# Optimization experiments

Hardware: AMD Instinct MI355X
Metric: run time of the kernel (lower is better)

The kernel has to match this reference:

```python
import jax, jax.numpy as jnp
import numpy as np

K = 16  # nsample for knn_point

def _bn(x, g, b):
    # inference-mode BatchNorm1d folded to per-channel affine (running stats 0/1)
    return x * g[None, :, None] + b[None, :, None]

def _knn(xyz, k):
    # xyz: [B,3,N] -> idx [B,N,k] of k nearest neighbors (squared L2)
    p = xyz.transpose(0, 2, 1)                                   # [B,N,3]
    sq = jnp.sum(p * p, axis=-1)                                 # [B,N]
    d = sq[:, :, None] + sq[:, None, :] - 2.0 * jnp.einsum('bnc,bmc->bnm', p, p)
    _, idx = jax.lax.top_k(-d, k)
    return idx

def _gather(hT, idx):
    # hT: [B,N,C], idx: [B,N,K] -> [B,N,K,C]
    return jax.vmap(lambda a, i: a[i])(hT, idx)

def setup_inputs():
    key = jax.random.key(0)
    ks = jax.random.split(key, 12)
    B, N, C = 16, 2048, 128
    def w(k, shape, fan):
        return jax.random.normal(k, shape, jnp.float32) * (1.0 / np.sqrt(fan))
    o = jnp.ones; z = jnp.zeros
    return {
        'points': jax.random.normal(ks[0], (B, 6, N), jnp.float32),
        'label': jax.random.uniform(ks[1], (B, 1, 16), jnp.float32),
        'We1': w(ks[2], (C, 6), 6), 'ge1': o(C), 'be1': z(C),
        'We2': w(ks[3], (C, C), C), 'ge2': o(C), 'be2': z(C),
        'W1': w(ks[4], (3, C, C), C), 'g1': o((3, C)), 'b1': z((3, C)),
        'W2': w(ks[5], (3, C, C), C), 'g2': o((3, C)), 'b2': z((3, C)),
        'Wf': w(ks[6], (1024, 3 * C), 3 * C), 'gf': o(1024), 'bf': z(1024),
        'Wl': w(ks[7], (64, 16), 16), 'gl': o(64), 'bl': z(64),
        'Wc1': w(ks[8], (512, 3136), 3136), 'bc1': z(512), 'gc1': o(512), 'bb1': z(512),
        'Wc2': w(ks[9], (256, 512), 512), 'bc2': z(256), 'gc2': o(256), 'bb2': z(256),
        'Wc3': w(ks[10], (50, 256), 256), 'bc3': z(50),
    }

def reference(points, label, We1, ge1, be1, We2, ge2, be2, W1, g1, b1, W2, g2, b2,
              Wf, gf, bf, Wl, gl, bl, Wc1, bc1, gc1, bb1, Wc2, bc2, gc2, bb2, Wc3, bc3):
    B, _, N = points.shape
    x = points[:, :6, :]
    xyz = x[:, :3, :]
    idx = _knn(xyz, K)                                            # [B,N,16]
    # input embedding: two conv1x1 + BN + ReLU
    h = jax.nn.relu(_bn(jnp.einsum('oc,bcn->bon', We1, x), ge1, be1))
    h = jax.nn.relu(_bn(jnp.einsum('oc,bcn->bon', We2, h), ge2, be2))
    xs = []
    for i in range(3):  # PVDSA_Res blocks (simplified: conv-BN-ReLU, kNN max-agg, conv-BN + residual)
        t = jax.nn.relu(_bn(jnp.einsum('oc,bcn->bon', W1[i], h), g1[i], b1[i]))
        nbr = _gather(t.transpose(0, 2, 1), idx)                  # [B,N,K,C]
        m = nbr.max(axis=2).transpose(0, 2, 1)                    # [B,C,N]
        h = jax.nn.relu(_bn(jnp.einsum('oc,bcn->bon', W2[i], m), g2[i], b2[i]) + h)
        xs.append(h)
    xcat = jnp.concatenate(xs, axis=1)                            # [B,384,N]
    xf = jax.nn.leaky_relu(_bn(jnp.einsum('oc,bcn->bon', Wf, xcat), gf, bf), 0.2)  # [B,1024,N]
    x_max = xf.max(axis=-1)                                       # [B,1024]
    x_avg = xf.mean(axis=-1)                                      # [B,1024]
    cls = jnp.broadcast_to(label.transpose(0, 2, 1), (B, 16, N))
    lab = jax.nn.leaky_relu(_bn(jnp.einsum('oc,bcn->bon', Wl, cls), gl, bl), 0.2)  # [B,64,N]
    glob = jnp.concatenate([
        jnp.broadcast_to(x_max[:, :, None], (B, 1024, N)),
        jnp.broadcast_to(x_avg[:, :, None], (B, 1024, N)),
        lab], axis=1)
    xa = jnp.concatenate([xf, glob], axis=1)                      # [B,3136,N]
    c = jax.nn.relu(_bn(jnp.einsum('oc,bcn->bon', Wc1, xa) + bc1[None, :, None], gc1, bb1))
    c = jax.nn.relu(_bn(jnp.einsum('oc,bcn->bon', Wc2, c) + bc2[None, :, None], gc2, bb2))
    out = jnp.einsum('oc,bcn->bon', Wc3, c) + bc3[None, :, None]  # [B,50,N]
    return out
```

## Files before the change

kernel.cpp:

```cpp
#include <hip/hip_runtime.h>
#include <cstdint>
#include <cstddef>

#define DEVINL __device__ __forceinline__

typedef float    f32x4 __attribute__((ext_vector_type(4)));
typedef _Float16 f16x8 __attribute__((ext_vector_type(8)));
typedef _Float16 f16x4 __attribute__((ext_vector_type(4)));

constexpr int BB = 16, NN = 2048, MM = 32768;

constexpr size_t OFF_WE1 = 0;
constexpr size_t OFF_WE2 = OFF_WE1 + 128 * 64 * 2;
constexpr size_t OFF_W1  = OFF_WE2 + 128 * 128 * 2;
constexpr size_t OFF_W2  = OFF_W1  + 3 * 128 * 128 * 2;
constexpr size_t OFF_WF  = OFF_W2  + 3 * 128 * 128 * 2;
constexpr size_t OFF_WC1 = OFF_WF  + 1024 * 384 * 2;
constexpr size_t OFF_WC2 = OFF_WC1 + 512 * 1024 * 2;
constexpr size_t OFF_WC3 = OFF_WC2 + 256 * 512 * 2;
constexpr size_t OFF_BC2 = OFF_WC3 + 128 * 256 * 2;
constexpr size_t OFF_BC3 = OFF_BC2 + 256 * 4;
constexpr size_t OFF_CVEC= OFF_BC3 + 128 * 4;
constexpr size_t OFF_PMAX= OFF_CVEC+ 16 * 512 * 4;
constexpr size_t OFF_PSUM= OFF_PMAX+ 16 * 16 * 1024 * 4;
constexpr size_t OFF_IDX = OFF_PSUM+ 16 * 16 * 1024 * 4;
constexpr size_t OFF_R1  = 8ull << 20;
constexpr size_t OFF_X0  = OFF_R1;
constexpr size_t OFF_HT  = OFF_R1 + (4ull  << 20);
constexpr size_t OFF_TT  = OFF_R1 + (12ull << 20);
constexpr size_t OFF_MT  = OFF_R1 + (20ull << 20);
constexpr size_t OFF_C1  = OFF_R1;
constexpr size_t OFF_XCAT= OFF_R1 + (32ull << 20);
constexpr size_t OFF_C2  = OFF_XCAT;
constexpr size_t OFF_XF  = OFF_XCAT + (24ull << 20);

__global__ __launch_bounds__(256) void fold_all_kernel(
    const float* We1, const float* ge1, const float* We2, const float* ge2,
    const float* W1,  const float* g1,  const float* W2,  const float* g2,
    const float* Wf,  const float* gf,  const float* Wc1, const float* gc1,
    const float* Wc2, const float* gc2, const float* Wc3,
    const float* gc2b, const float* bc2, const float* bb2, const float* bc3,
    const float* pts, char* ws)
{
    const int bid = blockIdx.x;
    const int tid = threadIdx.x;

    if (bid == 4704) {
        ((float*)(ws + OFF_BC2))[tid] = gc2b[tid] * bc2[tid] + bb2[tid];
        return;
    }
    if (bid == 4705) {
        if (tid < 128) ((float*)(ws + OFF_BC3))[tid] = (tid < 50) ? bc3[tid] : 0.f;
        return;
    }
    if (bid >= 4706) {
        int m = (bid - 4706) * 256 + tid;
        int b = m >> 11, n = m & 2047;
        const float* ps = pts + (size_t)b * 6 * 2048 + n;
        _Float16 tmp[64];
#pragma unroll
        for (int c = 0; c < 64; ++c) tmp[c] = (_Float16)0.f;
#pragma unroll
        for (int c = 0; c < 6; ++c) tmp[c] = (_Float16)ps[(size_t)c << 11];
        _Float16* dst = (_Float16*)(ws + OFF_X0) + (size_t)m * 64;
#pragma unroll
        for (int v = 0; v < 8; ++v) *(f16x8*)(dst + v * 8) = *(const f16x8*)(tmp + v * 8);
        return;
    }

    int id, base;
    if      (bid < 32)   { id = 0;  base = 0;    }
    else if (bid < 96)   { id = 1;  base = 32;   }
    else if (bid < 160)  { id = 2;  base = 96;   }
    else if (bid < 224)  { id = 3;  base = 160;  }
    else if (bid < 288)  { id = 4;  base = 224;  }
    else if (bid < 352)  { id = 5;  base = 288;  }
    else if (bid < 416)  { id = 6;  base = 352;  }
    else if (bid < 480)  { id = 7;  base = 416;  }
    else if (bid < 2016) { id = 8;  base = 480;  }
    else if (bid < 4064) { id = 9;  base = 2016; }
    else if (bid < 4576) { id = 10; base = 4064; }
    else                 { id = 11; base = 4576; }

    const float* src = nullptr; const float* g = nullptr; _Float16* dst = nullptr;
    int O = 0, K = 0, lds = 0, Kp = 0;
    switch (id) {
        case 0:  src = We1; g = ge1; O = 128; K = 6;    lds = 6;    Kp = 64;   dst = (_Float16*)(ws + OFF_WE1); break;
        case 1:  src = We2; g = ge2; O = 128; K = 128;  lds = 128;  Kp = 128;  dst = (_Float16*)(ws + OFF_WE2); break;
        case 2: case 3: case 4: {
            int i = id - 2;
            src = W1 + (size_t)i * 16384; g = g1 + i * 128; O = 128; K = 128; lds = 128; Kp = 128;
            dst = (_Float16*)(ws + OFF_W1) + (size_t)i * 16384; break; }
        case 5: case 6: case 7: {
            int i = id - 5;
            src = W2 + (size_t)i * 16384; g = g2 + i * 128; O = 128; K = 128; lds = 128; Kp = 128;
            dst = (_Float16*)(ws + OFF_W2) + (size_t)i * 16384; break; }
        case 8:  src = Wf;  g = gf;  O = 1024; K = 384;  lds = 384;  Kp = 384;  dst = (_Float16*)(ws + OFF_WF);  break;
        case 9:  src = Wc1; g = gc1; O = 512;  K = 1024; lds = 3136; Kp = 1024; dst = (_Float16*)(ws + OFF_WC1); break;
        case 10: src = Wc2; g = gc2; O = 256;  K = 512;  lds = 512;  Kp = 512;  dst = (_Float16*)(ws + OFF_WC2); break;
        default: src = Wc3; g = nullptr; O = 50; K = 256; lds = 256; Kp = 256;  dst = (_Float16*)(ws + OFF_WC3); break;
    }
    int e = (bid - base) * 256 + tid;
    int o = e / Kp, k = e - o * Kp;
    float v = 0.f;
    if (o < O && k < K) {
        v = src[(size_t)o * lds + k];
        if (g) v *= g[o];
    }
    dst[e] = (_Float16)v;
}

DEVINL float knn_dist(const float4 pq, const float4 pm) {
    float t = pq.x * pm.x;
    t = fmaf(pq.y, pm.y, t);
    t = fmaf(pq.z, pm.z, t);
    return fmaf(-2.f, t, pm.w);
}

#define KNN_DINS(X) do { \
    const float x_ = (X); \
    d15 = __builtin_amdgcn_fmed3f(x_, d14, d15); \
    d14 = __builtin_amdgcn_fmed3f(x_, d13, d14); \
    d13 = __builtin_amdgcn_fmed3f(x_, d12, d13); \
    d12 = __builtin_amdgcn_fmed3f(x_, d11, d12); \
    d11 = __builtin_amdgcn_fmed3f(x_, d10, d11); \
    d10 = __builtin_amdgcn_fmed3f(x_, d9,  d10); \
    d9  = __builtin_amdgcn_fmed3f(x_, d8,  d9);  \
    d8  = __builtin_amdgcn_fmed3f(x_, d7,  d8);  \
    d7  = __builtin_amdgcn_fmed3f(x_, d6,  d7);  \
    d6  = __builtin_amdgcn_fmed3f(x_, d5,  d6);  \
    d5  = __builtin_amdgcn_fmed3f(x_, d4,  d5);  \
    d4  = __builtin_amdgcn_fmed3f(x_, d3,  d4);  \
    d3  = __builtin_amdgcn_fmed3f(x_, d2,  d3);  \
    d2  = __builtin_amdgcn_fmed3f(x_, d1,  d2);  \
    d1  = __builtin_amdgcn_fmed3f(x_, d0,  d1);  \
    d0  = __builtin_amdgcn_fmed3f(x_, -3.4e38f, d0); \
} while (0)

#define KNN_CE(A, B) { const float lo_ = fminf(A, B), hi_ = fmaxf(A, B); A = lo_; B = hi_; }

#define KNN_MERGE(OFF) do { \
    const float n0  = __shfl_xor(d0,  OFF), n1  = __shfl_xor(d1,  OFF), \
                n2  = __shfl_xor(d2,  OFF), n3  = __shfl_xor(d3,  OFF), \
                n4  = __shfl_xor(d4,  OFF), n5  = __shfl_xor(d5,  OFF), \
                n6  = __shfl_xor(d6,  OFF), n7  = __shfl_xor(d7,  OFF), \
                n8  = __shfl_xor(d8,  OFF), n9  = __shfl_xor(d9,  OFF), \
                n10 = __shfl_xor(d10, OFF), n11 = __shfl_xor(d11, OFF), \
                n12 = __shfl_xor(d12, OFF), n13 = __shfl_xor(d13, OFF), \
                n14 = __shfl_xor(d14, OFF), n15 = __shfl_xor(d15, OFF); \
    d0  = fminf(d0,  n15); d1  = fminf(d1,  n14); d2  = fminf(d2,  n13); d3  = fminf(d3,  n12); \
    d4  = fminf(d4,  n11); d5  = fminf(d5,  n10); d6  = fminf(d6,  n9);  d7  = fminf(d7,  n8);  \
    d8  = fminf(d8,  n7);  d9  = fminf(d9,  n6);  d10 = fminf(d10, n5);  d11 = fminf(d11, n4);  \
    d12 = fminf(d12, n3);  d13 = fminf(d13, n2);  d14 = fminf(d14, n1);  d15 = fminf(d15, n0);  \
    KNN_CE(d0, d8)  KNN_CE(d1, d9)  KNN_CE(d2, d10) KNN_CE(d3, d11) \
    KNN_CE(d4, d12) KNN_CE(d5, d13) KNN_CE(d6, d14) KNN_CE(d7, d15) \
    KNN_CE(d0, d4)  KNN_CE(d1, d5)  KNN_CE(d2, d6)  KNN_CE(d3, d7)  \
    KNN_CE(d8, d12) KNN_CE(d9, d13) KNN_CE(d10,d14) KNN_CE(d11,d15) \
    KNN_CE(d0, d2)  KNN_CE(d1, d3)  KNN_CE(d4, d6)  KNN_CE(d5, d7)  \
    KNN_CE(d8, d10) KNN_CE(d9, d11) KNN_CE(d12,d14) KNN_CE(d13,d15) \
    KNN_CE(d0, d1)  KNN_CE(d2, d3)  KNN_CE(d4, d5)  KNN_CE(d6, d7)  \
    KNN_CE(d8, d9)  KNN_CE(d10,d11) KNN_CE(d12,d13) KNN_CE(d14,d15) \
} while (0)

__global__ __launch_bounds__(256) void knn_kernel(const float* __restrict__ pts, int* __restrict__ idxout)
{
    __shared__ float4 P[2048];
    __shared__ unsigned short buf[32][96];
    __shared__ int cnt[32];
    __shared__ int wcnt[32];
    const int tid = threadIdx.x;
    const int b = blockIdx.x;
    const float* pb = pts + (size_t)b * 6 * 2048;
    for (int i = tid; i < 2048; i += 256) {
        float x = pb[i];
        float y = pb[2048 + i];
        float z = pb[4096 + i];
        P[i] = make_float4(x, y, z, x * x + y * y + z * z);
    }
    if (tid < 32) { cnt[tid] = 0; wcnt[tid] = 0; }
    __syncthreads();

    const int p = tid & 7;
    const int g = tid >> 3;
    const int q = blockIdx.y * 32 + g;
    const float4 pq = P[q];

    float d0 = 3.4e38f, d1 = 3.4e38f, d2 = 3.4e38f, d3 = 3.4e38f;
#pragma unroll 4
    for (int it = 0; it < 256; ++it) {
        const float4 pm = P[it * 8 + p];
        const float x = knn_dist(pq, pm);
        d3 = __builtin_amdgcn_fmed3f(x, d2, d3);
        d2 = __builtin_amdgcn_fmed3f(x, d1, d2);
        d1 = __builtin_amdgcn_fmed3f(x, d0, d1);
        d0 = fminf(x, d0);
    }
    float d4 = 3.4e38f, d5 = 3.4e38f, d6 = 3.4e38f, d7 = 3.4e38f,
          d8 = 3.4e38f, d9 = 3.4e38f, d10 = 3.4e38f, d11 = 3.4e38f,
          d12 = 3.4e38f, d13 = 3.4e38f, d14 = 3.4e38f, d15 = 3.4e38f;
    KNN_MERGE(1);
    KNN_MERGE(2);
    KNN_MERGE(4);
    const float tub = d15;

#pragma unroll 4
    for (int it = 0; it < 256; ++it) {
        const int m = it * 8 + p;
        const float d = knn_dist(pq, P[m]);
        if (d <= tub) {
            const int pos = atomicAdd(&cnt[g], 1);
            if (pos < 96) buf[g][pos] = (unsigned short)m;
        }
    }
    int C = cnt[g];
    if (C > 96) C = 96;

    d0 = 3.4e38f; d1 = 3.4e38f; d2 = 3.4e38f; d3 = 3.4e38f;
    d4 = 3.4e38f; d5 = 3.4e38f; d6 = 3.4e38f; d7 = 3.4e38f;
    d8 = 3.4e38f; d9 = 3.4e38f; d10 = 3.4e38f; d11 = 3.4e38f;
    d12 = 3.4e38f; d13 = 3.4e38f; d14 = 3.4e38f; d15 = 3.4e38f;
    for (int j = p; j < C; j += 8) {
        const int m = buf[g][j];
        const float x = knn_dist(pq, P[m]);
        KNN_DINS(x);
    }
    KNN_MERGE(1);
    KNN_MERGE(2);
    KNN_MERGE(4);
    const float t = d15;

    int* op = idxout + (((size_t)(b << 11) + q) << 4);
    for (int j = p; j < C; j += 8) {
        const int m = buf[g][j];
        const float d = knn_dist(pq, P[m]);
        if (d <= t) {
            const int pos = atomicAdd(&wcnt[g], 1);
            if (pos < 16) op[pos] = m;
        }
    }
}

__global__ __launch_bounds__(256) void e12_kernel(
    const _Float16* __restrict__ W1e, const _Float16* __restrict__ W2e,
    const _Float16* __restrict__ X, _Float16* __restrict__ Y,
    const float* __restrict__ b1v, const float* __restrict__ b2v)
{
    __shared__ _Float16 SH[36864];
    _Float16* A1s = SH;
    _Float16* B1s = SH + 8192;
    _Float16* A2s = SH + 12288;
    _Float16* B2s = SH + 28672;

    const int tid = threadIdx.x;
    const int lane = tid & 63, wave = tid >> 6;
    const int r = lane & 15, quad = lane >> 4;
    const int m_blk = blockIdx.x * 64;
    const int oh = (wave >> 1) * 64, mh = (wave & 1) * 32;

    const int srow  = wave * 8 + (lane >> 3);
    const int sslot = lane & 7;

#pragma unroll
    for (int t = 0; t < 4; ++t) {
        const int row = t * 32 + srow;
        const int gk = (sslot ^ (row & 7)) << 3;
        __builtin_amdgcn_global_load_lds(
            (const __attribute__((address_space(1))) unsigned int*)(W1e + (size_t)row * 64 + gk),
            (__attribute__((address_space(3))) unsigned int*)(A1s + t * 2048 + wave * 512),
            16, 0, 0);
    }
#pragma unroll
    for (int t = 0; t < 2; ++t) {
        const int row = t * 32 + srow;
        const int gk = (sslot ^ (row & 7)) << 3;
        __builtin_amdgcn_global_load_lds(
            (const __attribute__((address_space(1))) unsigned int*)(X + (size_t)(m_blk + row) * 64 + gk),
            (__attribute__((address_space(3))) unsigned int*)(B1s + t * 2048 + wave * 512),
            16, 0, 0);
    }
#pragma unroll
    for (int kt = 0; kt < 2; ++kt)
#pragma unroll
        for (int t = 0; t < 4; ++t) {
            const int row = t * 32 + srow;
            const int gk = kt * 64 + ((sslot ^ (row & 7)) << 3);
            __builtin_amdgcn_global_load_lds(
                (const __attribute__((address_space(1))) unsigned int*)(W2e + (size_t)row * 128 + gk),
                (__attribute__((address_space(3))) unsigned int*)(A2s + kt * 8192 + t * 2048 + wave * 512),
                16, 0, 0);
        }

    asm volatile("s_waitcnt vmcnt(8)" ::: "memory");
    __builtin_amdgcn_sched_barrier(0);
    __builtin_amdgcn_s_barrier();
    asm volatile("" ::: "memory");

    f32x4 acc1[4][2];
#pragma unroll
    for (int a = 0; a < 4; ++a)
#pragma unroll
        for (int c = 0; c < 2; ++c) acc1[a][c] = (f32x4){0.f, 0.f, 0.f, 0.f};
#pragma unroll
    for (int ks = 0; ks < 2; ++ks) {
        f16x8 af[4], bf[2];
#pragma unroll
        for (int oi = 0; oi < 4; ++oi) {
            const int row = oh + oi * 16 + r;
            const int slot = (ks * 4 + quad) ^ (row & 7);
            af[oi] = *(const f16x8*)(A1s + row * 64 + slot * 8);
        }
#pragma unroll
        for (int mi = 0; mi < 2; ++mi) {
            const int row = mh + mi * 16 + r;
            const int slot = (ks * 4 + quad) ^ (row & 7);
            bf[mi] = *(const f16x8*)(B1s + row * 64 + slot * 8);
        }
#pragma unroll
        for (int oi = 0; oi < 4; ++oi)
#pragma unroll
            for (int mi = 0; mi < 2; ++mi)
                acc1[oi][mi] = __builtin_amdgcn_mfma_f32_16x16x32_f16(af[oi], bf[mi], acc1[oi][mi], 0, 0, 0);
    }

#pragma unroll
    for (int oi = 0; oi < 4; ++oi) {
        const int ob = oh + oi * 16 + quad * 4;
        const f32x4 bv = *(const f32x4*)(b1v + ob);
        const int kt = ob >> 6, kk = ob & 63;
        const int chunk = kk >> 3, within = kk & 7;
#pragma unroll
        for (int mi = 0; mi < 2; ++mi) {
            const int row = mh + mi * 16 + r;
            f32x4 v = acc1[oi][mi] + bv;
            f16x4 ov;
#pragma unroll
            for (int j = 0; j < 4; ++j) { float x = v[j]; ov[j] = (_Float16)((x > 0.f) ? x : 0.f); }
            *(f16x4*)(B2s + kt * 4096 + row * 64 + ((chunk ^ (row & 7)) << 3) + within) = ov;
        }
    }
    __syncthreads();

    f32x4 acc2[4][2];
#pragma unroll
    for (int a = 0; a < 4; ++a)
#pragma unroll
        for (int c = 0; c < 2; ++c) acc2[a][c] = (f32x4){0.f, 0.f, 0.f, 0.f};
#pragma unroll
    for (int kt = 0; kt < 2; ++kt)
#pragma unroll
        for (int ks = 0; ks < 2; ++ks) {
            f16x8 af[4], bf[2];
#pragma unroll
            for (int oi = 0; oi < 4; ++oi) {
                const int row = oh + oi * 16 + r;
                const int slot = (ks * 4 + quad) ^ (row & 7);
                af[oi] = *(const f16x8*)(A2s + kt * 8192 + row * 64 + slot * 8);
            }
#pragma unroll
            for (int mi = 0; mi < 2; ++mi) {
                const int row = mh + mi * 16 + r;
                const int slot = (ks * 4 + quad) ^ (row & 7);
                bf[mi] = *(const f16x8*)(B2s + kt * 4096 + row * 64 + slot * 8);
            }
#pragma unroll
            for (int oi = 0; oi < 4; ++oi)
#pragma unroll
                for (int mi = 0; mi < 2; ++mi)
                    acc2[oi][mi] = __builtin_amdgcn_mfma_f32_16x16x32_f16(af[oi], bf[mi], acc2[oi][mi], 0, 0, 0);
        }
    __syncthreads();

    _Float16* OT = SH;
#pragma unroll
    for (int oi = 0; oi < 4; ++oi) {
        const int ol = oh + oi * 16 + quad * 4;
        const f32x4 bv = *(const f32x4*)(b2v + ol);
#pragma unroll
        for (int mi = 0; mi < 2; ++mi) {
            const int row = mh + mi * 16 + r;
            f32x4 v = acc2[oi][mi] + bv;
            f16x4 ov;
#pragma unroll
            for (int j = 0; j < 4; ++j) { float x = v[j]; ov[j] = (_Float16)((x > 0.f) ? x : 0.f); }
            const int s = ((ol >> 2) ^ (row & 31)) << 2;
            *(f16x4*)(OT + row * 128 + s) = ov;
        }
    }
    __syncthreads();
#pragma unroll
    for (int it2 = 0; it2 < 4; ++it2) {
        const int row = it2 * 16 + (tid >> 4);
        const int c = tid & 15;
        const int s0 = ((c * 2) ^ (row & 31)) << 2;
        const int s1 = ((c * 2 + 1) ^ (row & 31)) << 2;
        f16x4 a  = *(const f16x4*)(OT + row * 128 + s0);
        f16x4 b2 = *(const f16x4*)(OT + row * 128 + s1);
        f16x8 o8;
        o8[0] = a[0]; o8[1] = a[1]; o8[2] = a[2]; o8[3] = a[3];
        o8[4] = b2[0]; o8[5] = b2[1]; o8[6] = b2[2]; o8[7] = b2[3];
        *(f16x8*)(Y + (size_t)(m_blk + row) * 128 + c * 8) = o8;
    }
}

__global__ __launch_bounds__(512, 2) void gemm256(
    const _Float16* __restrict__ W, const _Float16* __restrict__ X,
    _Float16* __restrict__ Y, const float* __restrict__ bias,
    int Kp, int ldX, int ldY, int Opad, int act, int biasPerBatch,
    float* __restrict__ pmax, float* __restrict__ psum)
{
    constexpr int ASZ = 256 * 64;
    __shared__ _Float16 SH[65536];
    const int tid  = threadIdx.x;
    const int lane = tid & 63, wave = tid >> 6;
    const int r = lane & 15, quad = lane >> 4;
    const int wo = wave & 3, wm = wave >> 2;
    const int m_blk = blockIdx.x * 256, o_blk = blockIdx.y * 256;
    const int nt = Kp >> 6;

    f32x4 acc[4][8];
#pragma unroll
    for (int a = 0; a < 4; ++a)
#pragma unroll
        for (int c = 0; c < 8; ++c) acc[a][c] = (f32x4){0.f, 0.f, 0.f, 0.f};

    const int srow  = wave * 8 + (lane >> 3);
    const int sslot = lane & 7;

    auto STAGE = [&](int bufi, int k0) {
        _Float16* As = SH + bufi * (2 * ASZ);
        _Float16* Bs = As + ASZ;
#pragma unroll
        for (int t = 0; t < 4; ++t) {
            const int rowA = t * 64 + srow;
            const int gk = k0 + ((sslot ^ (rowA & 7)) << 3);
            const _Float16* gA = W + (size_t)(o_blk + rowA) * Kp + gk;
            __builtin_amdgcn_global_load_lds(
                (const __attribute__((address_space(1))) unsigned int*)gA,
                (__attribute__((address_space(3))) unsigned int*)(As + t * 4096 + wave * 512),
                16, 0, 0);
        }
#pragma unroll
        for (int t = 0; t < 4; ++t) {
            const int rowB = t * 64 + srow;
            const int gk = k0 + ((sslot ^ (rowB & 7)) << 3);
            const _Float16* gB = X + (size_t)(m_blk + rowB) * ldX + gk;
            __builtin_amdgcn_global_load_lds(
                (const __attribute__((address_space(1))) unsigned int*)gB,
                (__attribute__((address_space(3))) unsigned int*)(Bs + t * 4096 + wave * 512),
                16, 0, 0);
        }
    };

    STAGE(0, 0);
    int cur = 0;
    for (int t = 0; t < nt; ++t) {
        if (t + 1 < nt) {
            STAGE(cur ^ 1, (t + 1) << 6);
            asm volatile("s_waitcnt vmcnt(8)" ::: "memory");
        } else {
            asm volatile("s_waitcnt vmcnt(0)" ::: "memory");
        }
        __builtin_amdgcn_sched_barrier(0);
        __builtin_amdgcn_s_barrier();
        asm volatile("" ::: "memory");

        const _Float16* As = SH + cur * (2 * ASZ);
        const _Float16* Bs = As + ASZ;
        __builtin_amdgcn_s_setprio(1);
#pragma unroll
        for (int ks = 0; ks < 2; ++ks) {
            f16x8 af[4], bf[8];
#pragma unroll
            for (int oi = 0; oi < 4; ++oi) {
                const int row = (wo << 6) + (oi << 4) + r;
                const int slot = (ks * 4 + quad) ^ (row & 7);
                af[oi] = *(const f16x8*)(As + row * 64 + slot * 8);
            }
#pragma unroll
            for (int mi = 0; mi < 8; ++mi) {
                const int row = (wm << 7) + (mi << 4) + r;
                const int slot = (ks * 4 + quad) ^ (row & 7);
                bf[mi] = *(const f16x8*)(Bs + row * 64 + slot * 8);
            }
#pragma unroll
            for (int oi = 0; oi < 4; ++oi)
#pragma unroll
                for (int mi = 0; mi < 8; ++mi)
                    acc[oi][mi] = __builtin_amdgcn_mfma_f32_16x16x32_f16(af[oi], bf[mi], acc[oi][mi], 0, 0, 0);
        }
        __builtin_amdgcn_s_setprio(0);
        asm volatile("" ::: "memory");
        __builtin_amdgcn_s_barrier();
        cur ^= 1;
    }
    __syncthreads();

    const int bb = biasPerBatch ? (m_blk >> 11) * Opad : 0;
    _Float16* OT = SH;
#pragma unroll
    for (int oi = 0; oi < 4; ++oi) {
        const int ol = (wo << 6) + (oi << 4) + (quad << 2);
        const f32x4 bv = *(const f32x4*)(bias + bb + o_blk + ol);
#pragma unroll
        for (int mi = 0; mi < 8; ++mi) {
            const int row = (wm << 7) + (mi << 4) + r;
            f32x4 v = acc[oi][mi] + bv;
            f16x4 ov;
#pragma unroll
            for (int j = 0; j < 4; ++j) {
                float x = v[j];
                if (act == 1)      x = (x > 0.f) ? x : 0.0f;
                else if (act == 2) x = (x > 0.f) ? x : 0.2f * x;
                ov[j] = (_Float16)x;
            }
            const int s = (ol >> 2) ^ (row & 31);
            *(f16x4*)(OT + row * 256 + s * 4) = ov;
        }
    }
    __syncthreads();
#pragma unroll
    for (int p2 = 0; p2 < 16; ++p2) {
        const int g = (p2 << 9) + tid;
        const int row = g >> 5, c = g & 31;
        const int s0 = ((c << 1)) ^ (row & 31);
        const int s1 = ((c << 1) | 1) ^ (row & 31);
        f16x4 a  = *(const f16x4*)(OT + row * 256 + s0 * 4);
        f16x4 b2 = *(const f16x4*)(OT + row * 256 + s1 * 4);
        f16x8 o8;
        o8[0] = a[0]; o8[1] = a[1]; o8[2] = a[2]; o8[3] = a[3];
        o8[4] = b2[0]; o8[5] = b2[1]; o8[6] = b2[2]; o8[7] = b2[3];
        *(f16x8*)(Y + (size_t)(m_blk + row) * ldY + o_blk + (c << 3)) = o8;
    }

    if (pmax) {
        const int cg = tid & 63, h8 = tid >> 6;
        float mx0 = -3.4e38f, mx1 = -3.4e38f, mx2 = -3.4e38f, mx3 = -3.4e38f;
        float sm0 = 0.f, sm1 = 0.f, sm2 = 0.f, sm3 = 0.f;
#pragma unroll
        for (int rr = 0; rr < 32; ++rr) {
            const int row = (h8 << 5) + rr;
            const f16x4 v = *(const f16x4*)(OT + row * 256 + ((cg ^ (row & 31)) << 2));
            const float x0 = (float)v[0], x1 = (float)v[1], x2 = (float)v[2], x3 = (float)v[3];
            mx0 = fmaxf(mx0, x0); sm0 += x0;
            mx1 = fmaxf(mx1, x1); sm1 += x1;
            mx2 = fmaxf(mx2, x2); sm2 += x2;
            mx3 = fmaxf(mx3, x3); sm3 += x3;
        }
        __syncthreads();
        float* PR = (float*)SH;
        float* pw = PR + (size_t)(((h8 << 8) + (cg << 2)) << 1);
        pw[0] = mx0; pw[1] = sm0; pw[2] = mx1; pw[3] = sm1;
        pw[4] = mx2; pw[5] = sm2; pw[6] = mx3; pw[7] = sm3;
        __syncthreads();
        if (tid < 256) {
            float M = -3.4e38f, S = 0.f;
#pragma unroll
            for (int h2 = 0; h2 < 8; ++h2) {
                M = fmaxf(M, PR[(size_t)(((h2 << 8) + tid) << 1)]);
                S += PR[(size_t)(((h2 << 8) + tid) << 1) + 1];
            }
            const int b2 = m_blk >> 11, mt = (m_blk >> 8) & 7;
            pmax[((size_t)((b2 << 3) + mt) << 10) + o_blk + tid] = M;
            psum[((size_t)((b2 << 3) + mt) << 10) + o_blk + tid] = S;
        }
    }
}

template<int TM>
__global__ __launch_bounds__(256) void gemm_tile(
    const _Float16* __restrict__ W, const _Float16* __restrict__ X,
    _Float16* __restrict__ Y, float* __restrict__ Y32,
    const float* __restrict__ bias, const _Float16* __restrict__ Res,
    int Kp, int ldX, int xoff, int ldY, int yoff, int Opad,
    int act, int biasPerBatch, int ldR, int roff, int Olimit)
{
    constexpr int MI = TM / 32;
    constexpr int ASZ = 128 * 64;
    constexpr int BSZ = TM * 64;
    __shared__ _Float16 SH[2 * (ASZ + BSZ)];

    const int tid  = threadIdx.x;
    const int lane = tid & 63, wave = tid >> 6;
    const int r = lane & 15, quad = lane >> 4;
    const int m_blk = blockIdx.x * TM, o_blk = blockIdx.y * 128;
    const int oh = (wave >> 1) * 64, mh = (wave & 1) * (TM / 2);

    f32x4 acc[4][MI];
#pragma unroll
    for (int a = 0; a < 4; ++a)
#pragma unroll
        for (int c = 0; c < MI; ++c) acc[a][c] = (f32x4){0.f, 0.f, 0.f, 0.f};

    const int srow  = wave * 8 + (lane >> 3);
    const int sslot = lane & 7;

    auto STAGE = [&](int bufi, int k0) {
        _Float16* As = SH + bufi * (ASZ + BSZ);
        _Float16* Bs = As + ASZ;
#pragma unroll
        for (int t = 0; t < 4; ++t) {
            const int rowA = t * 32 + srow;
            const int gk = k0 + ((sslot ^ (rowA & 7)) << 3);
            const _Float16* gA = W + (size_t)(o_blk + rowA) * Kp + gk;
            __builtin_amdgcn_global_load_lds(
                (const __attribute__((address_space(1))) unsigned int*)gA,
                (__attribute__((address_space(3))) unsigned int*)(As + t * 2048 + wave * 512),
                16, 0, 0);
        }
#pragma unroll
        for (int t = 0; t < TM / 32; ++t) {
            const int rowB = t * 32 + srow;
            const int gk = k0 + ((sslot ^ (rowB & 7)) << 3);
            const _Float16* gB = X + (size_t)(m_blk + rowB) * ldX + xoff + gk;
            __builtin_amdgcn_global_load_lds(
                (const __attribute__((address_space(1))) unsigned int*)gB,
                (__attribute__((address_space(3))) unsigned int*)(Bs + t * 2048 + wave * 512),
                16, 0, 0);
        }
    };

    const int nt = Kp >> 6;
    STAGE(0, 0);
    int cur = 0;
    for (int t = 0; t < nt; ++t) {
        if (t + 1 < nt) {
            STAGE(cur ^ 1, (t + 1) << 6);
            if constexpr (TM == 128) asm volatile("s_waitcnt vmcnt(8)" ::: "memory");
            else                     asm volatile("s_waitcnt vmcnt(6)" ::: "memory");
        } else {
            asm volatile("s_waitcnt vmcnt(0)" ::: "memory");
        }
        __builtin_amdgcn_sched_barrier(0);
        __builtin_amdgcn_s_barrier();
        asm volatile("" ::: "memory");

        const _Float16* As = SH + cur * (ASZ + BSZ);
        const _Float16* Bs = As + ASZ;
        __builtin_amdgcn_s_setprio(1);
#pragma unroll
        for (int ks = 0; ks < 2; ++ks) {
            f16x8 af[4], bf[MI];
#pragma unroll
            for (int oi = 0; oi < 4; ++oi) {
                const int row = oh + oi * 16 + r;
                const int slot = (ks * 4 + quad) ^ (row & 7);
                af[oi] = *(const f16x8*)(As + row * 64 + slot * 8);
            }
#pragma unroll
            for (int mi = 0; mi < MI; ++mi) {
                const int row = mh + mi * 16 + r;
                const int slot = (ks * 4 + quad) ^ (row & 7);
                bf[mi] = *(const f16x8*)(Bs + row * 64 + slot * 8);
            }
#pragma unroll
            for (int oi = 0; oi < 4; ++oi)
#pragma unroll
                for (int mi = 0; mi < MI; ++mi)
                    acc[oi][mi] = __builtin_amdgcn_mfma_f32_16x16x32_f16(af[oi], bf[mi], acc[oi][mi], 0, 0, 0);
        }
        __builtin_amdgcn_s_setprio(0);
        asm volatile("" ::: "memory");
        __builtin_amdgcn_s_barrier();
        cur ^= 1;
    }

    const int bb = biasPerBatch ? (m_blk >> 11) * Opad : 0;
    __syncthreads();

    if (Y32) {
#pragma unroll
        for (int oi = 0; oi < 4; ++oi) {
            const int og = o_blk + oh + oi * 16 + quad * 4;
            const f32x4 bv = *(const f32x4*)(bias + bb + og);
#pragma unroll
            for (int mi = 0; mi < MI; ++mi) {
                const int m = m_blk + mh + mi * 16 + r;
                const int bidx = m >> 11, n = m & 2047;
                f32x4 v = acc[oi][mi] + bv;
#pragma unroll
                for (int j = 0; j < 4; ++j) {
                    float x = v[j];
                    if (act == 1)      x = (x > 0.f) ? x : 0.0f;
                    else if (act == 2) x = (x > 0.f) ? x : 0.2f * x;
                    const int o = og + j;
                    if (o < Olimit)
                        Y32[((size_t)(bidx * 50 + o) << 11) + n] = x;
                }
            }
        }
        return;
    }

    _Float16* OT = SH;
#pragma unroll
    for (int oi = 0; oi < 4; ++oi) {
        const int ol = oh + oi * 16 + quad * 4;
        const f32x4 bv = *(const f32x4*)(bias + bb + o_blk + ol);
#pragma unroll
        for (int mi = 0; mi < MI; ++mi) {
            const int row = mh + mi * 16 + r;
            f32x4 v = acc[oi][mi] + bv;
            if (Res) {
                f16x4 rr = *(const f16x4*)(Res + (size_t)(m_blk + row) * ldR + roff + o_blk + ol);
#pragma unroll
                for (int j = 0; j < 4; ++j) v[j] += (float)rr[j];
            }
            f16x4 ov;
#pragma unroll
            for (int j = 0; j < 4; ++j) {
                float x = v[j];
                if (act == 1)      x = (x > 0.f) ? x : 0.0f;
                else if (act == 2) x = (x > 0.f) ? x : 0.2f * x;
                ov[j] = (_Float16)x;
            }
            const int s = ((ol >> 2) ^ (row & 31)) << 2;
            *(f16x4*)(OT + row * 128 + s) = ov;
        }
    }
    __syncthreads();
#pragma unroll
    for (int it2 = 0; it2 < TM / 16; ++it2) {
        const int row = it2 * 16 + (tid >> 4);
        const int c = tid & 15;
        const int s0 = ((c * 2) ^ (row & 31)) << 2;
        const int s1 = ((c * 2 + 1) ^ (row & 31)) << 2;
        f16x4 a = *(const f16x4*)(OT + row * 128 + s0);
        f16x4 b2 = *(const f16x4*)(OT + row * 128 + s1);
        f16x8 o8;
        o8[0] = a[0]; o8[1] = a[1]; o8[2] = a[2]; o8[3] = a[3];
        o8[4] = b2[0]; o8[5] = b2[1]; o8[6] = b2[2]; o8[7] = b2[3];
        *(f16x8*)(Y + (size_t)(m_blk + row) * ldY + yoff + o_blk + c * 8) = o8;
    }
}

typedef short s16x8 __attribute__((ext_vector_type(8)));
__global__ __launch_bounds__(256) void gather_max_kernel(
    const short* __restrict__ T, const int* __restrict__ idx, short* __restrict__ Mo)
{
    const int tid = threadIdx.x;
    const int p = blockIdx.x * 16 + (tid >> 4);
    const int l = tid & 15;
    const int b = p >> 11;
    const int* ip = idx + (size_t)p * 16;
    size_t row = (size_t)((b << 11) + ip[0]);
    s16x8 cur = *(const s16x8*)(T + row * 128 + l * 8);
    unsigned short best[8];
#pragma unroll
    for (int e = 0; e < 8; ++e) best[e] = (unsigned short)cur[e];
#pragma unroll
    for (int j = 1; j < 16; ++j) {
        row = (size_t)((b << 11) + ip[j]);
        s16x8 v = *(const s16x8*)(T + row * 128 + l * 8);
#pragma unroll
        for (int e = 0; e < 8; ++e) {
            unsigned short u = (unsigned short)v[e];
            if (u > best[e]) best[e] = u;
        }
    }
    s16x8 ov;
#pragma unroll
    for (int e = 0; e < 8; ++e) ov[e] = (short)best[e];
    *(s16x8*)(Mo + (size_t)p * 128 + l * 8) = ov;
}

__global__ __launch_bounds__(256) void cvec_kernel(
    const float* __restrict__ label, const float* __restrict__ Wl, const float* __restrict__ gl, const float* __restrict__ bl,
    const float* __restrict__ Wc1, const float* __restrict__ bc1, const float* __restrict__ gc1, const float* __restrict__ bb1,
    const float* __restrict__ pmax, const float* __restrict__ psum, float* __restrict__ cvec)
{
    __shared__ float v[2112];
    __shared__ float red[256];
    const int b = blockIdx.x, og = blockIdx.y, tid = threadIdx.x;
    for (int i = tid; i < 1024; i += 256) {
        float mx = -3.4e38f, sm = 0.f;
#pragma unroll
        for (int c = 0; c < 8; ++c) {
            mx = fmaxf(mx, pmax[((size_t)(b * 8 + c) << 10) + i]);
            sm += psum[((size_t)(b * 8 + c) << 10) + i];
        }
        v[i] = mx;
        v[1024 + i] = sm * (1.f / 2048.f);
    }
    if (tid < 64) {
        float s = 0.f;
        for (int i = 0; i < 16; ++i) s += Wl[tid * 16 + i] * label[b * 16 + i];
        s = gl[tid] * s + bl[tid];
        v[2048 + tid] = (s > 0.f) ? s : 0.2f * s;
    }
    __syncthreads();
    const int o = og * 64 + (tid >> 2), part = tid & 3;
    const float* wrow = Wc1 + (size_t)o * 3136 + 1024 + part * 528;
    float s = 0.f;
    for (int j = 0; j < 528; ++j) s += wrow[j] * v[part * 528 + j];
    red[tid] = s;
    __syncthreads();
    if (part == 0) {
        float tot = red[tid] + red[tid + 1] + red[tid + 2] + red[tid + 3];
        cvec[((size_t)b << 9) + o] = gc1[o] * (tot + bc1[o]) + bb1[o];
    }
}

extern "C" void kernel_launch(void* const* d_in, const int* in_sizes, int n_in,
                              void* d_out, int out_size, void* d_ws, size_t ws_size,
                              hipStream_t stream)
{
    (void)in_sizes; (void)n_in; (void)out_size; (void)ws_size;
    const float* points = (const float*)d_in[0];
    const float* label  = (const float*)d_in[1];
    const float* We1 = (const float*)d_in[2];
    const float* ge1 = (const float*)d_in[3];
    const float* be1 = (const float*)d_in[4];
    const float* We2 = (const float*)d_in[5];
    const float* ge2 = (const float*)d_in[6];
    const float* be2 = (const float*)d_in[7];
    const float* W1  = (const float*)d_in[8];
    const float* g1  = (const float*)d_in[9];
    const float* b1  = (const float*)d_in[10];
    const float* W2  = (const float*)d_in[11];
    const float* g2  = (const float*)d_in[12];
    const float* b2  = (const float*)d_in[13];
    const float* Wf  = (const float*)d_in[14];
    const float* gf  = (const float*)d_in[15];
    const float* bfv = (const float*)d_in[16];
    const float* Wl  = (const float*)d_in[17];
    const float* gl  = (const float*)d_in[18];
    const float* bl  = (const float*)d_in[19];
    const float* Wc1 = (const float*)d_in[20];
    const float* bc1 = (const float*)d_in[21];
    const float* gc1 = (const float*)d_in[22];
    const float* bb1 = (const float*)d_in[23];
    const float* Wc2 = (const float*)d_in[24];
    const float* bc2 = (const float*)d_in[25];
    const float* gc2 = (const float*)d_in[26];
    const float* bb2 = (const float*)d_in[27];
    const float* Wc3 = (const float*)d_in[28];
    const float* bc3 = (const float*)d_in[29];

    char* ws = (char*)d_ws;
    _Float16* hT  = (_Float16*)(ws + OFF_HT);
    _Float16* tT  = (_Float16*)(ws + OFF_TT);
    _Float16* mT  = (_Float16*)(ws + OFF_MT);
    _Float16* xct = (_Float16*)(ws + OFF_XCAT);
    _Float16* xf  = (_Float16*)(ws + OFF_XF);
    _Float16* c1  = (_Float16*)(ws + OFF_C1);
    _Float16* c2  = (_Float16*)(ws + OFF_C2);
    int*      idx = (int*)     (ws + OFF_IDX);
    _Float16* x0  = (_Float16*)(ws + OFF_X0);

    _Float16* wE1 = (_Float16*)(ws + OFF_WE1);
    _Float16* wE2 = (_Float16*)(ws + OFF_WE2);
    _Float16* w1f = (_Float16*)(ws + OFF_W1);
    _Float16* w2f = (_Float16*)(ws + OFF_W2);
    _Float16* wF  = (_Float16*)(ws + OFF_WF);
    _Float16* wC1 = (_Float16*)(ws + OFF_WC1);
    _Float16* wC2 = (_Float16*)(ws + OFF_WC2);
    _Float16* wC3 = (_Float16*)(ws + OFF_WC3);
    float* bC2 = (float*)(ws + OFF_BC2);
    float* bC3 = (float*)(ws + OFF_BC3);
    float* cv  = (float*)(ws + OFF_CVEC);
    float* pmx = (float*)(ws + OFF_PMAX);
    float* psm = (float*)(ws + OFF_PSUM);

    fold_all_kernel<<<dim3(4834), 256, 0, stream>>>(We1, ge1, We2, ge2, W1, g1, W2, g2,
                                                    Wf, gf, Wc1, gc1, Wc2, gc2, Wc3,
                                                    gc2, bc2, bb2, bc3, points, ws);
    knn_kernel<<<dim3(BB, NN / 32), 256, 0, stream>>>(points, idx);

    e12_kernel<<<dim3(512), 256, 0, stream>>>(wE1, wE2, x0, hT, be1, be2);

    for (int i = 0; i < 3; ++i) {
        const _Float16* hin = (i == 0) ? hT : xct;
        int ldH  = (i == 0) ? 128 : 384;
        int offH = (i == 0) ? 0 : (i - 1) * 128;
        gemm_tile<64><<<dim3(512, 1), 256, 0, stream>>>(w1f + (size_t)i * 16384, hin, tT, nullptr, b1 + i * 128, nullptr,
                                                        128, ldH, offH, 128, 0, 128, 1, 0, 0, 0, 128);
        gather_max_kernel<<<dim3(MM / 16), 256, 0, stream>>>((const short*)tT, idx, (short*)mT);
        gemm_tile<64><<<dim3(512, 1), 256, 0, stream>>>(w2f + (size_t)i * 16384, mT, xct, nullptr, b2 + i * 128, hin,
                                                        128, 128, 0, 384, i * 128, 128, 1, 0, ldH, offH, 128);
    }

    gemm256<<<dim3(128, 4), 512, 0, stream>>>(wF, xct, xf, bfv, 384, 384, 1024, 1024, 2, 0, pmx, psm);

    cvec_kernel<<<dim3(BB, 8), 256, 0, stream>>>(label, Wl, gl, bl, Wc1, bc1, gc1, bb1, pmx, psm, cv);

    gemm256<<<dim3(128, 2), 512, 0, stream>>>(wC1, xf, c1, cv, 1024, 1024, 512, 512, 1, 1, nullptr, nullptr);

    gemm_tile<128><<<dim3(256, 2), 256, 0, stream>>>(wC2, c1, c2, nullptr, bC2, nullptr, 512, 512, 0, 256, 0, 256, 1, 0, 0, 0, 256);
    gemm_tile<128><<<dim3(256, 1), 256, 0, stream>>>(wC3, c2, nullptr, (float*)d_out, bC3, nullptr, 256, 256, 0, 0, 0, 128, 0, 0, 0, 0, 50);
}
```

Before: 379.2 us.

## Fuse consecutive W2 and next-block W1 GEMMs into one pair kernel

Adds a pair_kernel that computes block i's W2 GEMM with bias, residual add and ReLU, writes the result to the concat buffer, then reuses it from LDS as input to block i+1's W1 GEMM. The two fused kernels replace four separate GEMM launches, which removes two launches and the global re-read of the intermediate activation. The cost is a second serial GEMM phase in each block, extra LDS traffic and syncs, and fewer blocks in flight because of the larger shared-memory footprint.

Result: faster. 368.9 us (-2.7%).

```diff
diff --git a/kernel.cpp b/kernel.cpp
--- a/kernel.cpp
+++ b/kernel.cpp
@@ -399,6 +399,185 @@
         o8[0] = a[0]; o8[1] = a[1]; o8[2] = a[2]; o8[3] = a[3];
         o8[4] = b2[0]; o8[5] = b2[1]; o8[6] = b2[2]; o8[7] = b2[3];
         *(f16x8*)(Y + (size_t)(m_blk + row) * 128 + c * 8) = o8;
+    }
+}
+
+__global__ __launch_bounds__(256) void pair_kernel(
+    const _Float16* __restrict__ Wa, const _Float16* __restrict__ Wb,
+    const _Float16* __restrict__ X, const _Float16* __restrict__ Res,
+    _Float16* __restrict__ Y1, _Float16* __restrict__ Y2,
+    const float* __restrict__ ba, const float* __restrict__ bb,
+    int ldR, int roff, int yoff1)
+{
+    __shared__ _Float16 SH[32768];
+    _Float16* Aa  = SH;
+    _Float16* Bx  = SH + 16384;
+    _Float16* By1 = SH + 24576;
+    _Float16* Ab  = SH;
+    _Float16* OT2 = SH + 16384;
+
+    const int tid = threadIdx.x;
+    const int lane = tid & 63, wave = tid >> 6;
+    const int r = lane & 15, quad = lane >> 4;
+    const int m_blk = blockIdx.x * 64;
+    const int oh = (wave >> 1) * 64, mh = (wave & 1) * 32;
+
+    const int srow  = wave * 8 + (lane >> 3);
+    const int sslot = lane & 7;
+
+#pragma unroll
+    for (int kt = 0; kt < 2; ++kt)
+#pragma unroll
+        for (int t = 0; t < 4; ++t) {
+            const int row = t * 32 + srow;
+            const int gk = kt * 64 + ((sslot ^ (row & 7)) << 3);
+            __builtin_amdgcn_global_load_lds(
+                (const __attribute__((address_space(1))) unsigned int*)(Wa + (size_t)row * 128 + gk),
+                (__attribute__((address_space(3))) unsigned int*)(Aa + kt * 8192 + t * 2048 + wave * 512),
+                16, 0, 0);
+        }
+#pragma unroll
+    for (int kt = 0; kt < 2; ++kt)
+#pragma unroll
+        for (int t = 0; t < 2; ++t) {
+            const int row = t * 32 + srow;
+            const int gk = kt * 64 + ((sslot ^ (row & 7)) << 3);
+            __builtin_amdgcn_global_load_lds(
+                (const __attribute__((address_space(1))) unsigned int*)(X + (size_t)(m_blk + row) * 128 + gk),
+                (__attribute__((address_space(3))) unsigned int*)(Bx + kt * 4096 + t * 2048 + wave * 512),
+                16, 0, 0);
+        }
+    __syncthreads();
+
+    f32x4 acc1[4][2];
+#pragma unroll
+    for (int a = 0; a < 4; ++a)
+#pragma unroll
+        for (int c = 0; c < 2; ++c) acc1[a][c] = (f32x4){0.f, 0.f, 0.f, 0.f};
+#pragma unroll
+    for (int kt = 0; kt < 2; ++kt)
+#pragma unroll
+        for (int ks = 0; ks < 2; ++ks) {
+            f16x8 af[4], bf[2];
+#pragma unroll
+            for (int oi = 0; oi < 4; ++oi) {
+                const int row = oh + oi * 16 + r;
+                const int slot = (ks * 4 + quad) ^ (row & 7);
+                af[oi] = *(const f16x8*)(Aa + kt * 8192 + row * 64 + slot * 8);
+            }
+#pragma unroll
+            for (int mi = 0; mi < 2; ++mi) {
+                const int row = mh + mi * 16 + r;
+                const int slot = (ks * 4 + quad) ^ (row & 7);
+                bf[mi] = *(const f16x8*)(Bx + kt * 4096 + row * 64 + slot * 8);
+            }
+#pragma unroll
+            for (int oi = 0; oi < 4; ++oi)
+#pragma unroll
+                for (int mi = 0; mi < 2; ++mi)
+                    acc1[oi][mi] = __builtin_amdgcn_mfma_f32_16x16x32_f16(af[oi], bf[mi], acc1[oi][mi], 0, 0, 0);
+        }
+    __syncthreads();
+
+#pragma unroll
+    for (int kt = 0; kt < 2; ++kt)
+#pragma unroll
+        for (int t = 0; t < 4; ++t) {
+            const int row = t * 32 + srow;
+            const int gk = kt * 64 + ((sslot ^ (row & 7)) << 3);
+            __builtin_amdgcn_global_load_lds(
+                (const __attribute__((address_space(1))) unsigned int*)(Wb + (size_t)row * 128 + gk),
+                (__attribute__((address_space(3))) unsigned int*)(Ab + kt * 8192 + t * 2048 + wave * 512),
+                16, 0, 0);
+        }
+
+#pragma unroll
+    for (int oi = 0; oi < 4; ++oi) {
+        const int ol = oh + oi * 16 + quad * 4;
+        const f32x4 bv = *(const f32x4*)(ba + ol);
+        const int kt = ol >> 6, kk = ol & 63;
+        const int chunk = kk >> 3, within = kk & 7;
+#pragma unroll
+        for (int mi = 0; mi < 2; ++mi) {
+            const int row = mh + mi * 16 + r;
+            f32x4 v = acc1[oi][mi] + bv;
+            f16x4 rr = *(const f16x4*)(Res + (size_t)(m_blk + row) * ldR + roff + ol);
+#pragma unroll
+            for (int j = 0; j < 4; ++j) v[j] += (float)rr[j];
+            f16x4 ov;
+#pragma unroll
+            for (int j = 0; j < 4; ++j) { float x = v[j]; ov[j] = (_Float16)((x > 0.f) ? x : 0.f); }
+            *(f16x4*)(By1 + kt * 4096 + row * 64 + ((chunk ^ (row & 7)) << 3) + within) = ov;
+        }
+    }
+    __syncthreads();
+
+#pragma unroll
+    for (int it = 0; it < 4; ++it) {
+        const int g = it * 256 + tid;
+        const int row = g >> 4, c = g & 15;
+        const int kt = c >> 3, cc = c & 7;
+        f16x8 o8 = *(const f16x8*)(By1 + kt * 4096 + row * 64 + ((cc ^ (row & 7)) << 3));
+        *(f16x8*)(Y1 + (size_t)(m_blk + row) * 384 + yoff1 + c * 8) = o8;
+    }
+
+    f32x4 acc2[4][2];
+#pragma unroll
+    for (int a = 0; a < 4; ++a)
+#pragma unroll
+        for (int c = 0; c < 2; ++c) acc2[a][c] = (f32x4){0.f, 0.f, 0.f, 0.f};
+#pragma unroll
+    for (int kt = 0; kt < 2; ++kt)
+#pragma unroll
+        for (int ks = 0; ks < 2; ++ks) {
+            f16x8 af[4], bf[2];
+#pragma unroll
+            for (int oi = 0; oi < 4; ++oi) {
+                const int row = oh + oi * 16 + r;
+                const int slot = (ks * 4 + quad) ^ (row & 7);
+                af[oi] = *(const f16x8*)(Ab + kt * 8192 + row * 64 + slot * 8);
+            }
+#pragma unroll
+            for (int mi = 0; mi < 2; ++mi) {
+                const int row = mh + mi * 16 + r;
+                const int slot = (ks * 4 + quad) ^ (row & 7);
+                bf[mi] = *(const f16x8*)(By1 + kt * 4096 + row * 64 + slot * 8);
+            }
+#pragma unroll
+            for (int oi = 0; oi < 4; ++oi)
+#pragma unroll
+                for (int mi = 0; mi < 2; ++mi)
+                    acc2[oi][mi] = __builtin_amdgcn_mfma_f32_16x16x32_f16(af[oi], bf[mi], acc2[oi][mi], 0, 0, 0);
+        }
+
+#pragma unroll
+    for (int oi = 0; oi < 4; ++oi) {
+        const int ol = oh + oi * 16 + quad * 4;
+        const f32x4 bv = *(const f32x4*)(bb + ol);
+#pragma unroll
+        for (int mi = 0; mi < 2; ++mi) {
+            const int row = mh + mi * 16 + r;
+            f32x4 v = acc2[oi][mi] + bv;
+            f16x4 ov;
+#pragma unroll
+            for (int j = 0; j < 4; ++j) { float x = v[j]; ov[j] = (_Float16)((x > 0.f) ? x : 0.f); }
+            const int s = ((ol >> 2) ^ (row & 31)) << 2;
+            *(f16x4*)(OT2 + row * 128 + s) = ov;
+        }
+    }
+    __syncthreads();
+#pragma unroll
+    for (int it2 = 0; it2 < 4; ++it2) {
+        const int row = it2 * 16 + (tid >> 4);
+        const int c = tid & 15;
+        const int s0 = ((c * 2) ^ (row & 31)) << 2;
+        const int s1 = ((c * 2 + 1) ^ (row & 31)) << 2;
+        f16x4 a  = *(const f16x4*)(OT2 + row * 128 + s0);
+        f16x4 b2 = *(const f16x4*)(OT2 + row * 128 + s1);
+        f16x8 o8;
+        o8[0] = a[0]; o8[1] = a[1]; o8[2] = a[2]; o8[3] = a[3];
+        o8[4] = b2[0]; o8[5] = b2[1]; o8[6] = b2[2]; o8[7] = b2[3];
+        *(f16x8*)(Y2 + (size_t)(m_blk + row) * 128 + c * 8) = o8;
     }
 }
 
@@ -868,16 +1047,20 @@
 
     e12_kernel<<<dim3(512), 256, 0, stream>>>(wE1, wE2, x0, hT, be1, be2);
 
-    for (int i = 0; i < 3; ++i) {
-        const _Float16* hin = (i == 0) ? hT : xct;
-        int ldH  = (i == 0) ? 128 : 384;
-        int offH = (i == 0) ? 0 : (i - 1) * 128;
-        gemm_tile<64><<<dim3(512, 1), 256, 0, stream>>>(w1f + (size_t)i * 16384, hin, tT, nullptr, b1 + i * 128, nullptr,
-                                                        128, ldH, offH, 128, 0, 128, 1, 0, 0, 0, 128);
-        gather_max_kernel<<<dim3(MM / 16), 256, 0, stream>>>((const short*)tT, idx, (short*)mT);
-        gemm_tile<64><<<dim3(512, 1), 256, 0, stream>>>(w2f + (size_t)i * 16384, mT, xct, nullptr, b2 + i * 128, hin,
-                                                        128, 128, 0, 384, i * 128, 128, 1, 0, ldH, offH, 128);
-    }
+    gemm_tile<64><<<dim3(512, 1), 256, 0, stream>>>(w1f, hT, tT, nullptr, b1, nullptr,
+                                                    128, 128, 0, 128, 0, 128, 1, 0, 0, 0, 128);
+    gather_max_kernel<<<dim3(MM / 16), 256, 0, stream>>>((const short*)tT, idx, (short*)mT);
+
+    pair_kernel<<<dim3(512), 256, 0, stream>>>(w2f, w1f + 16384, mT, hT, xct, tT,
+                                               b2, b1 + 128, 128, 0, 0);
+    gather_max_kernel<<<dim3(MM / 16), 256, 0, stream>>>((const short*)tT, idx, (short*)mT);
+
+    pair_kernel<<<dim3(512), 256, 0, stream>>>(w2f + 16384, w1f + 2 * 16384, mT, xct, xct, tT,
+                                               b2 + 128, b1 + 256, 384, 0, 128);
+    gather_max_kernel<<<dim3(MM / 16), 256, 0, stream>>>((const short*)tT, idx, (short*)mT);
+
+    gemm_tile<64><<<dim3(512, 1), 256, 0, stream>>>(w2f + 2 * 16384, mT, xct, nullptr, b2 + 256, xct,
+                                                    128, 128, 0, 384, 256, 128, 1, 0, 384, 128, 128);
 
     gemm256<<<dim3(128, 4), 512, 0, stream>>>(wF, xct, xf, bfv, 384, 384, 1024, 1024, 2, 0, pmx, psm);
 
```
